# Optimization experiments

Hardware: AMD Instinct MI355X
Metric: run time of the kernel (lower is better)

Reference implementation:

```python
import jax, jax.numpy as jnp
import numpy as np

X_SCALE, X_ZP = 0.03, -66      # int8 quant params (qmin=-128, qmax=127)
Y_SCALE, Y_ZP = 0.025, 160     # uint8 quant params (qmin=0, qmax=255)
M = K = N = 4096


def setup_inputs() -> dict:
    key = jax.random.key(0)
    kx, ky = jax.random.split(key)
    # x holds int8-range values [-128, 127], y holds uint8-range values [0, 255]
    x = jax.random.randint(kx, (M, K), -128, 128, dtype=jnp.int32)
    y = jax.random.randint(ky, (K, N), 0, 256, dtype=jnp.int32)
    return {"x": x, "y": y}


def reference(x, y):
    # dequantize_per_tensor: (q - zero_point) * scale  (values already in [qmin, qmax])
    xf = (x.astype(jnp.float32) - X_ZP) * X_SCALE   # [M, K]
    yf = (y.astype(jnp.float32) - Y_ZP) * Y_SCALE   # [K, N]
    return jnp.matmul(xf, yf)                       # [M, N]
```

## Files before the change

### kernel.cpp

```cpp
#include <hip/hip_runtime.h>
#include <stdint.h>

#define Mdim 4096
#define Kdim 4096
#define Ndim 4096

typedef __attribute__((ext_vector_type(4))) int v4i;
typedef __attribute__((ext_vector_type(16))) int v16i;

__device__ __forceinline__ void gload_lds16(const void* g, void* l) {
  __builtin_amdgcn_global_load_lds(
      (__attribute__((address_space(1))) void*)(uintptr_t)g,
      (__attribute__((address_space(3))) void*)(uint32_t)(uintptr_t)l,
      16, 0, 0);
}

__global__ __launch_bounds__(256) void pack_x_kernel(const int* __restrict__ x,
                                                     char* __restrict__ x8,
                                                     int* __restrict__ rsx) {
  const int row = blockIdx.x;
  const int t = threadIdx.x;
  const int4* src = (const int4*)(x + (size_t)row * Kdim) + t * 4;
  int sum = 0;
  int p[4];
#pragma unroll
  for (int i = 0; i < 4; ++i) {
    int4 v = src[i];
    sum += v.x + v.y + v.z + v.w;
    p[i] = (v.x & 0xff) | ((v.y & 0xff) << 8) | ((v.z & 0xff) << 16) | (v.w << 24);
  }
  ((int4*)x8)[(size_t)row * 256 + t] = make_int4(p[0], p[1], p[2], p[3]);
#pragma unroll
  for (int o = 32; o > 0; o >>= 1) sum += __shfl_down(sum, o, 64);
  __shared__ int red[4];
  if ((t & 63) == 0) red[t >> 6] = sum;
  __syncthreads();
  if (t == 0) rsx[row] = red[0] + red[1] + red[2] + red[3];
}

__global__ __launch_bounds__(256) void pack_yt_kernel(const int* __restrict__ y,
                                                      char* __restrict__ yt) {
  __shared__ char tile[64][68];
  const int t = threadIdx.x;
  const int n0 = blockIdx.x * 64;
  const int k0 = blockIdx.y * 64;
  const int c = t & 63;
  const int r4 = t >> 6;
#pragma unroll
  for (int it = 0; it < 16; ++it) {
    const int r = it * 4 + r4;
    const int v = y[(size_t)(k0 + r) * Ndim + n0 + c];
    tile[c][r] = (char)(v - 128);
  }
  __syncthreads();
  const int orow = t >> 4;
  const int ocb = (t & 15) * 4;
#pragma unroll
  for (int it = 0; it < 4; ++it) {
    const int rr = it * 16 + orow;
    int wv = (tile[rr][ocb] & 0xff) | ((tile[rr][ocb + 1] & 0xff) << 8) |
             ((tile[rr][ocb + 2] & 0xff) << 16) | (tile[rr][ocb + 3] << 24);
    *(int*)(yt + (size_t)(n0 + rr) * Kdim + k0 + ocb) = wv;
  }
}

__global__ __launch_bounds__(256) void colsum_kernel(const char* __restrict__ yt,
                                                     int* __restrict__ csy) {
  const int n = blockIdx.x;
  const int t = threadIdx.x;
  int4 v = ((const int4*)yt)[(size_t)n * 256 + t];
  int words[4] = {v.x, v.y, v.z, v.w};
  int s = 0;
#pragma unroll
  for (int i = 0; i < 4; ++i) {
    int w = words[i];
    s += (int)(char)(w) + (int)(char)(w >> 8) + (int)(char)(w >> 16) + (w >> 24);
  }
#pragma unroll
  for (int o = 32; o > 0; o >>= 1) s += __shfl_down(s, o, 64);
  __shared__ int red[4];
  if ((t & 63) == 0) red[t >> 6] = s;
  __syncthreads();
  if (t == 0) csy[n] = red[0] + red[1] + red[2] + red[3];
}

__global__ __launch_bounds__(256) void gemm_i8_kernel(
    const char* __restrict__ A, const char* __restrict__ B,
    const int* __restrict__ rsx, const int* __restrict__ csy,
    float* __restrict__ out) {
  __shared__ __align__(16) char As[128 * 64];
  __shared__ __align__(16) char Bs[128 * 64];
  const int t = threadIdx.x;
  const int l = t & 63;
  const int w = t >> 6;
  const int wr = w >> 1;
  const int wc = w & 1;
  const int bm = blockIdx.y * 128;
  const int bn = blockIdx.x * 128;

  v16i acc[2][2];
#pragma unroll
  for (int i = 0; i < 2; ++i)
#pragma unroll
    for (int j = 0; j < 2; ++j)
#pragma unroll
      for (int q = 0; q < 16; ++q) acc[i][j][q] = 0;

  const int srow = t >> 2;
  const int cswz = (t & 3) ^ (srow & 3);
  const char* gA = A + (size_t)(bm + srow) * Kdim + cswz * 16;
  const char* gB = B + (size_t)(bn + srow) * Kdim + cswz * 16;
  char* lA = As + t * 16;
  char* lB = Bs + t * 16;

  const int am = wr * 64 + (l & 31);
  const int bnr = wc * 64 + (l & 31);
  const int lhalf = l >> 5;
  const int lswz = l & 3;

  for (int kt = 0; kt < 64; ++kt) {
    const int koff = kt * 64;
    gload_lds16(gA + koff, lA);
    gload_lds16(gA + koff + (size_t)64 * Kdim, lA + 64 * 64);
    gload_lds16(gB + koff, lB);
    gload_lds16(gB + koff + (size_t)64 * Kdim, lB + 64 * 64);
    __syncthreads();
#pragma unroll
    for (int ks = 0; ks < 2; ++ks) {
      const int c0 = ((ks * 2 + lhalf) ^ lswz) * 16;
      v4i a0 = *(const v4i*)(As + (am)*64 + c0);
      v4i a1 = *(const v4i*)(As + (am + 32) * 64 + c0);
      v4i b0 = *(const v4i*)(Bs + (bnr)*64 + c0);
      v4i b1 = *(const v4i*)(Bs + (bnr + 32) * 64 + c0);
      acc[0][0] = __builtin_amdgcn_mfma_i32_32x32x32_i8(a0, b0, acc[0][0], 0, 0, 0);
      acc[0][1] = __builtin_amdgcn_mfma_i32_32x32x32_i8(a0, b1, acc[0][1], 0, 0, 0);
      acc[1][0] = __builtin_amdgcn_mfma_i32_32x32x32_i8(a1, b0, acc[1][0], 0, 0, 0);
      acc[1][1] = __builtin_amdgcn_mfma_i32_32x32x32_i8(a1, b1, acc[1][1], 0, 0, 0);
    }
    __syncthreads();
  }

  const int col = l & 31;
#pragma unroll
  for (int i = 0; i < 2; ++i) {
#pragma unroll
    for (int j = 0; j < 2; ++j) {
      const int gm0 = bm + wr * 64 + i * 32;
      const int gn = bn + wc * 64 + j * 32 + col;
      const int cs = 66 * csy[gn] - 8650752;
#pragma unroll
      for (int r = 0; r < 16; ++r) {
        const int row = (r & 3) + 8 * (r >> 2) + 4 * lhalf;
        const int gm = gm0 + row;
        const int val = acc[i][j][r] - 32 * rsx[gm] + cs;
        out[(size_t)gm * Ndim + gn] = 7.5e-4f * (float)val;
      }
    }
  }
}

extern "C" void kernel_launch(void* const* d_in, const int* in_sizes, int n_in,
                              void* d_out, int out_size, void* d_ws, size_t ws_size,
                              hipStream_t stream) {
  (void)in_sizes; (void)n_in; (void)out_size; (void)ws_size;
  const int* x = (const int*)d_in[0];
  const int* y = (const int*)d_in[1];
  float* out = (float*)d_out;
  char* ws = (char*)d_ws;
  char* x8 = ws;
  char* yt = ws + (size_t)Mdim * Kdim;
  int* rsx = (int*)(ws + (size_t)Mdim * Kdim + (size_t)Kdim * Ndim);
  int* csy = rsx + Mdim;

  pack_x_kernel<<<Mdim, 256, 0, stream>>>(x, x8, rsx);
  pack_yt_kernel<<<dim3(Ndim / 64, Kdim / 64), 256, 0, stream>>>(y, yt);
  colsum_kernel<<<Ndim, 256, 0, stream>>>(yt, csy);
  gemm_i8_kernel<<<dim3(Ndim / 128, Mdim / 128), 256, 0, stream>>>(x8, yt, rsx, csy, out);
}
```

Measured before the change: 270.5 us.

## Enlarge GEMM tiles to 256x256 with LDS double buffering and fuse column sums

The int8 GEMM tile grows from 128x128 to 256x256 per block, with a 4x4 grid of MFMA accumulators per wave and a double-buffered LDS pipeline that prefetches the next K-slice while computing the current one. The y transpose/pack kernel now also computes column sums, using atomics into a zeroed buffer, which removes the separate colsum kernel launch and its reread of yt. The changes aim to raise data reuse per LDS load and to hide global-load latency. In exchange they add register pressure (256 accumulator VGPRs, occupancy 1) and leave only 256 blocks, which risks load imbalance across CUs.

```diff
diff --git a/kernel.cpp b/kernel.cpp
--- a/kernel.cpp
+++ b/kernel.cpp
@@ -39,114 +39,116 @@
 }
 
 __global__ __launch_bounds__(256) void pack_yt_kernel(const int* __restrict__ y,
-                                                      char* __restrict__ yt) {
-  __shared__ char tile[64][68];
+                                                      char* __restrict__ yt,
+                                                      int* __restrict__ csy) {
+  __shared__ int wtile[64 * 24];
+  __shared__ int psum[4][64];
   const int t = threadIdx.x;
   const int n0 = blockIdx.x * 64;
   const int k0 = blockIdx.y * 64;
-  const int c = t & 63;
-  const int r4 = t >> 6;
-#pragma unroll
-  for (int it = 0; it < 16; ++it) {
-    const int r = it * 4 + r4;
-    const int v = y[(size_t)(k0 + r) * Ndim + n0 + c];
-    tile[c][r] = (char)(v - 128);
-  }
-  __syncthreads();
-  const int orow = t >> 4;
-  const int ocb = (t & 15) * 4;
+  const int nl = t & 63;
+  const int rq = t >> 6;
+  int s = 0;
 #pragma unroll
   for (int it = 0; it < 4; ++it) {
-    const int rr = it * 16 + orow;
-    int wv = (tile[rr][ocb] & 0xff) | ((tile[rr][ocb + 1] & 0xff) << 8) |
-             ((tile[rr][ocb + 2] & 0xff) << 16) | (tile[rr][ocb + 3] << 24);
-    *(int*)(yt + (size_t)(n0 + rr) * Kdim + k0 + ocb) = wv;
+    const int q = rq + it * 4;
+    int v0 = y[(size_t)(k0 + q * 4 + 0) * Ndim + n0 + nl];
+    int v1 = y[(size_t)(k0 + q * 4 + 1) * Ndim + n0 + nl];
+    int v2 = y[(size_t)(k0 + q * 4 + 2) * Ndim + n0 + nl];
+    int v3 = y[(size_t)(k0 + q * 4 + 3) * Ndim + n0 + nl];
+    v0 -= 128; v1 -= 128; v2 -= 128; v3 -= 128;
+    s += v0 + v1 + v2 + v3;
+    wtile[nl * 24 + q] = (v0 & 0xff) | ((v1 & 0xff) << 8) | ((v2 & 0xff) << 16) | (v3 << 24);
+  }
+  psum[rq][nl] = s;
+  __syncthreads();
+  const int orow = t >> 2;
+  const int cw = t & 3;
+  int4 wv = *(const int4*)(wtile + orow * 24 + cw * 4);
+  *(int4*)(yt + (size_t)(n0 + orow) * Kdim + k0 + cw * 16) = wv;
+  if (t < 64) {
+    int tot = psum[0][t] + psum[1][t] + psum[2][t] + psum[3][t];
+    atomicAdd(csy + n0 + t, tot);
   }
 }
 
-__global__ __launch_bounds__(256) void colsum_kernel(const char* __restrict__ yt,
-                                                     int* __restrict__ csy) {
-  const int n = blockIdx.x;
-  const int t = threadIdx.x;
-  int4 v = ((const int4*)yt)[(size_t)n * 256 + t];
-  int words[4] = {v.x, v.y, v.z, v.w};
-  int s = 0;
-#pragma unroll
-  for (int i = 0; i < 4; ++i) {
-    int w = words[i];
-    s += (int)(char)(w) + (int)(char)(w >> 8) + (int)(char)(w >> 16) + (w >> 24);
-  }
-#pragma unroll
-  for (int o = 32; o > 0; o >>= 1) s += __shfl_down(s, o, 64);
-  __shared__ int red[4];
-  if ((t & 63) == 0) red[t >> 6] = s;
-  __syncthreads();
-  if (t == 0) csy[n] = red[0] + red[1] + red[2] + red[3];
-}
-
-__global__ __launch_bounds__(256) void gemm_i8_kernel(
+__global__ __launch_bounds__(256, 1) void gemm_i8_kernel(
     const char* __restrict__ A, const char* __restrict__ B,
     const int* __restrict__ rsx, const int* __restrict__ csy,
     float* __restrict__ out) {
-  __shared__ __align__(16) char As[128 * 64];
-  __shared__ __align__(16) char Bs[128 * 64];
+  __shared__ __align__(16) char lds[2 * 32768];
   const int t = threadIdx.x;
   const int l = t & 63;
   const int w = t >> 6;
   const int wr = w >> 1;
   const int wc = w & 1;
-  const int bm = blockIdx.y * 128;
-  const int bn = blockIdx.x * 128;
+  const int bm = blockIdx.y * 256;
+  const int bn = blockIdx.x * 256;
 
-  v16i acc[2][2];
+  v16i acc[4][4];
 #pragma unroll
-  for (int i = 0; i < 2; ++i)
+  for (int i = 0; i < 4; ++i)
 #pragma unroll
-    for (int j = 0; j < 2; ++j)
+    for (int j = 0; j < 4; ++j)
 #pragma unroll
       for (int q = 0; q < 16; ++q) acc[i][j][q] = 0;
 
   const int srow = t >> 2;
-  const int cswz = (t & 3) ^ (srow & 3);
-  const char* gA = A + (size_t)(bm + srow) * Kdim + cswz * 16;
-  const char* gB = B + (size_t)(bn + srow) * Kdim + cswz * 16;
-  char* lA = As + t * 16;
-  char* lB = Bs + t * 16;
+  const int cswz = ((t & 3) ^ ((t >> 3) & 3)) * 16;
+  const char* gA = A + (size_t)(bm + srow) * Kdim + cswz;
+  const char* gB = B + (size_t)(bn + srow) * Kdim + cswz;
 
-  const int am = wr * 64 + (l & 31);
-  const int bnr = wc * 64 + (l & 31);
+#define STAGE(buf_off, koff)                                                  \
+  do {                                                                        \
+    _Pragma("unroll") for (int i = 0; i < 4; ++i)                             \
+        gload_lds16(gA + (koff) + (size_t)i * 64 * Kdim,                      \
+                    lds + (buf_off) + i * 4096 + t * 16);                     \
+    _Pragma("unroll") for (int i = 0; i < 4; ++i)                             \
+        gload_lds16(gB + (koff) + (size_t)i * 64 * Kdim,                      \
+                    lds + (buf_off) + 16384 + i * 4096 + t * 16);             \
+  } while (0)
+
+  const int arow = wr * 128 + (l & 31);
+  const int brow = wc * 128 + (l & 31);
   const int lhalf = l >> 5;
-  const int lswz = l & 3;
+  const int lkey = (l >> 1) & 3;
 
-  for (int kt = 0; kt < 64; ++kt) {
-    const int koff = kt * 64;
-    gload_lds16(gA + koff, lA);
-    gload_lds16(gA + koff + (size_t)64 * Kdim, lA + 64 * 64);
-    gload_lds16(gB + koff, lB);
-    gload_lds16(gB + koff + (size_t)64 * Kdim, lB + 64 * 64);
+#define COMPUTE(buf_off)                                                      \
+  do {                                                                        \
+    const char* As = lds + (buf_off);                                         \
+    const char* Bs = lds + (buf_off) + 16384;                                 \
+    _Pragma("unroll") for (int ks = 0; ks < 2; ++ks) {                        \
+      const int slot = ((ks * 2 + lhalf) ^ lkey) * 16;                        \
+      v4i a[4], b[4];                                                         \
+      _Pragma("unroll") for (int i = 0; i < 4; ++i)                           \
+          a[i] = *(const v4i*)(As + (arow + i * 32) * 64 + slot);             \
+      _Pragma("unroll") for (int j = 0; j < 4; ++j)                           \
+          b[j] = *(const v4i*)(Bs + (brow + j * 32) * 64 + slot);             \
+      _Pragma("unroll") for (int i = 0; i < 4; ++i)                           \
+          _Pragma("unroll") for (int j = 0; j < 4; ++j)                       \
+              acc[i][j] = __builtin_amdgcn_mfma_i32_32x32x32_i8(              \
+                  a[i], b[j], acc[i][j], 0, 0, 0);                            \
+    }                                                                         \
+  } while (0)
+
+  STAGE(0, 0);
+  __syncthreads();
+  for (int kt = 0; kt < 64; kt += 2) {
+    if (kt + 1 < 64) STAGE(32768, (kt + 1) * 64);
+    COMPUTE(0);
     __syncthreads();
-#pragma unroll
-    for (int ks = 0; ks < 2; ++ks) {
-      const int c0 = ((ks * 2 + lhalf) ^ lswz) * 16;
-      v4i a0 = *(const v4i*)(As + (am)*64 + c0);
-      v4i a1 = *(const v4i*)(As + (am + 32) * 64 + c0);
-      v4i b0 = *(const v4i*)(Bs + (bnr)*64 + c0);
-      v4i b1 = *(const v4i*)(Bs + (bnr + 32) * 64 + c0);
-      acc[0][0] = __builtin_amdgcn_mfma_i32_32x32x32_i8(a0, b0, acc[0][0], 0, 0, 0);
-      acc[0][1] = __builtin_amdgcn_mfma_i32_32x32x32_i8(a0, b1, acc[0][1], 0, 0, 0);
-      acc[1][0] = __builtin_amdgcn_mfma_i32_32x32x32_i8(a1, b0, acc[1][0], 0, 0, 0);
-      acc[1][1] = __builtin_amdgcn_mfma_i32_32x32x32_i8(a1, b1, acc[1][1], 0, 0, 0);
-    }
+    if (kt + 2 < 64) STAGE(0, (kt + 2) * 64);
+    COMPUTE(32768);
     __syncthreads();
   }
 
   const int col = l & 31;
 #pragma unroll
-  for (int i = 0; i < 2; ++i) {
+  for (int i = 0; i < 4; ++i) {
+    const int gm0 = bm + wr * 128 + i * 32;
 #pragma unroll
-    for (int j = 0; j < 2; ++j) {
-      const int gm0 = bm + wr * 64 + i * 32;
-      const int gn = bn + wc * 64 + j * 32 + col;
+    for (int j = 0; j < 4; ++j) {
+      const int gn = bn + wc * 128 + j * 32 + col;
       const int cs = 66 * csy[gn] - 8650752;
 #pragma unroll
       for (int r = 0; r < 16; ++r) {
@@ -157,6 +159,8 @@
       }
     }
   }
+#undef STAGE
+#undef COMPUTE
 }
 
 extern "C" void kernel_launch(void* const* d_in, const int* in_sizes, int n_in,
@@ -172,8 +176,8 @@
   int* rsx = (int*)(ws + (size_t)Mdim * Kdim + (size_t)Kdim * Ndim);
   int* csy = rsx + Mdim;
 
+  hipMemsetAsync(csy, 0, Ndim * sizeof(int), stream);
   pack_x_kernel<<<Mdim, 256, 0, stream>>>(x, x8, rsx);
-  pack_yt_kernel<<<dim3(Ndim / 64, Kdim / 64), 256, 0, stream>>>(y, yt);
-  colsum_kernel<<<Ndim, 256, 0, stream>>>(yt, csy);
-  gemm_i8_kernel<<<dim3(Ndim / 128, Mdim / 128), 256, 0, stream>>>(x8, yt, rsx, csy, out);
+  pack_yt_kernel<<<dim3(Ndim / 64, Kdim / 64), 256, 0, stream>>>(y, yt, csy);
+  gemm_i8_kernel<<<dim3(Ndim / 256, Mdim / 256), 256, 0, stream>>>(x8, yt, rsx, csy, out);
 }
```

Measured after the change: 256.9 us. 5.0% less time.
